# Kernel optimization log

Hardware: AMD Instinct MI355X
Metric: run time of the kernel (lower is better)

Reference implementation:

```python
import jax, jax.numpy as jnp
import numpy as np

NUM_HEADS = 32
NUM_KV_HEADS = 8
HEAD_DIM = 128
HIDDEN = 4096
ROPE_THETA = 10000.0
NEG = -1e9


def _split_heads(x, num_heads):
    b, s, _ = x.shape
    return x.reshape(b, s, num_heads, HEAD_DIM).transpose(0, 2, 1, 3)  # (B,H,S,D)


def _rope_cos_sin(position_ids, dtype):
    # position_ids: (B, S) int
    inv_freq = 1.0 / (ROPE_THETA ** (jnp.arange(0, HEAD_DIM, 2, dtype=jnp.float32) / HEAD_DIM))
    freqs = position_ids.astype(jnp.float32)[..., None] * inv_freq  # (B,S,D/2)
    emb = jnp.concatenate([freqs, freqs], axis=-1)  # (B,S,D)
    return jnp.cos(emb).astype(dtype)[:, None], jnp.sin(emb).astype(dtype)[:, None]  # (B,1,S,D)


def _rotate_half(x):
    x1, x2 = jnp.split(x, 2, axis=-1)
    return jnp.concatenate([-x2, x1], axis=-1)


def setup_inputs() -> dict:
    key = jax.random.key(0)
    ks = jax.random.split(key, 6)
    B, S = 1, 2048
    hidden_states = jax.random.normal(ks[0], (B, S, HIDDEN), dtype=jnp.float32)
    # additive causal mask: 0 on/below diagonal, NEG above
    causal = jnp.triu(jnp.full((S, S), NEG, dtype=jnp.float32), k=1)
    attention_mask = jnp.broadcast_to(causal, (B, 1, S, S))
    position_ids = jnp.broadcast_to(jnp.arange(S, dtype=jnp.int32), (B, S))
    sd = 1.0 / np.sqrt(HIDDEN)
    Wq = jax.random.normal(ks[1], (HIDDEN, NUM_HEADS * HEAD_DIM), dtype=jnp.float32) * sd
    Wk = jax.random.normal(ks[2], (HIDDEN, NUM_KV_HEADS * HEAD_DIM), dtype=jnp.float32) * sd
    Wv = jax.random.normal(ks[3], (HIDDEN, NUM_KV_HEADS * HEAD_DIM), dtype=jnp.float32) * sd
    Wo = jax.random.normal(ks[4], (NUM_HEADS * HEAD_DIM, HIDDEN), dtype=jnp.float32) * sd
    return {"hidden_states": hidden_states, "attention_mask": attention_mask,
            "position_ids": position_ids, "Wq": Wq, "Wk": Wk, "Wv": Wv, "Wo": Wo}


def reference(hidden_states, attention_mask, position_ids, Wq, Wk, Wv, Wo):
    groups = NUM_HEADS // NUM_KV_HEADS
    scale = HEAD_DIM ** (-0.5)
    q = _split_heads(hidden_states @ Wq, NUM_HEADS)        # (B,H,S,D)
    k = _split_heads(hidden_states @ Wk, NUM_KV_HEADS)     # (B,Hkv,S,D)
    v = _split_heads(hidden_states @ Wv, NUM_KV_HEADS)
    cos, sin = _rope_cos_sin(position_ids, q.dtype)
    q = q * cos + _rotate_half(q) * sin
    k = k * cos + _rotate_half(k) * sin
    # repeat_kv (faithful to tf.repeat along head axis)
    k = jnp.repeat(k, groups, axis=1)                      # (B,H,S,D)
    v = jnp.repeat(v, groups, axis=1)
    attn = jnp.einsum('bhqd,bhkd->bhqk', q, k) * scale
    attn = attn + attention_mask.astype(attn.dtype)
    attn = jax.nn.softmax(attn.astype(jnp.float32), axis=-1).astype(q.dtype)
    out = jnp.einsum('bhqk,bhkd->bhqd', attn, v)           # (B,H,S,D)
    b, _, s, _ = out.shape
    out = out.transpose(0, 2, 1, 3).reshape(b, s, NUM_HEADS * HEAD_DIM)
    return out @ Wo
```

## Files before the change

kernel.cpp:

```cpp
#include <hip/hip_runtime.h>
#include <math.h>

#define S_LEN 2048
#define HIDDEN 4096
#define NUM_HEADS 32
#define NUM_KV_HEADS 8
#define HEAD_DIM 128
#define NEG (-1e9f)

using short8 = __attribute__((ext_vector_type(8))) short;
using f32x4 = __attribute__((ext_vector_type(4))) float;

__device__ inline unsigned short f2bf(float f) {
  union { float f; unsigned u; } c;
  c.f = f;
  unsigned r = c.u + 0x7fffu + ((c.u >> 16) & 1u);
  return (unsigned short)(r >> 16);
}
__device__ inline float bf2f(unsigned short h) {
  union { unsigned u; float f; } c;
  c.u = ((unsigned)h) << 16;
  return c.f;
}
__device__ inline void gload16(const void* g, void* l) {
  __builtin_amdgcn_global_load_lds(
      (const __attribute__((address_space(1))) unsigned*)g,
      (__attribute__((address_space(3))) unsigned*)l, 16, 0, 0);
}

__global__ __launch_bounds__(256) void split_mat(const float* __restrict__ X,
                                                 unsigned short* __restrict__ Xh,
                                                 unsigned short* __restrict__ Xl,
                                                 int n4) {
  const int i = blockIdx.x * 256 + threadIdx.x;
  if (i >= n4) return;
  const float4 x = *reinterpret_cast<const float4*>(&X[(size_t)i * 4]);
  ushort4 h, l;
  h.x = f2bf(x.x); l.x = f2bf(x.x - bf2f(h.x));
  h.y = f2bf(x.y); l.y = f2bf(x.y - bf2f(h.y));
  h.z = f2bf(x.z); l.z = f2bf(x.z - bf2f(h.z));
  h.w = f2bf(x.w); l.w = f2bf(x.w - bf2f(h.w));
  *reinterpret_cast<ushort4*>(&Xh[(size_t)i * 4]) = h;
  *reinterpret_cast<ushort4*>(&Xl[(size_t)i * 4]) = l;
}

__global__ __launch_bounds__(256) void split_transpose(
    const float* __restrict__ B, unsigned short* __restrict__ Th,
    unsigned short* __restrict__ Tl, int K, int N) {
  __shared__ float ts[32][33];
  const int t = threadIdx.x;
  const int k0 = blockIdx.y * 32, n0 = blockIdx.x * 32;
  const int r = t >> 3, c4 = (t & 7) << 2;
  const float4 x = *reinterpret_cast<const float4*>(&B[(size_t)(k0 + r) * N + n0 + c4]);
  ts[r][c4 + 0] = x.x;
  ts[r][c4 + 1] = x.y;
  ts[r][c4 + 2] = x.z;
  ts[r][c4 + 3] = x.w;
  __syncthreads();
  const int col = r, ks = c4;
  ushort4 h, l;
#pragma unroll
  for (int e = 0; e < 4; ++e) {
    const float v = ts[ks + e][col];
    const unsigned short hh = f2bf(v);
    const unsigned short ll = f2bf(v - bf2f(hh));
    ((unsigned short*)&h)[e] = hh;
    ((unsigned short*)&l)[e] = ll;
  }
  *reinterpret_cast<ushort4*>(&Th[(size_t)(n0 + col) * K + k0 + ks]) = h;
  *reinterpret_cast<ushort4*>(&Tl[(size_t)(n0 + col) * K + k0 + ks]) = l;
}

#define BM 128
#define BN 128
#define BK 32

__global__ __launch_bounds__(256) void gemm_split(
    const unsigned short* __restrict__ Ah, const unsigned short* __restrict__ Al,
    const unsigned short* __restrict__ Bh, const unsigned short* __restrict__ Bl,
    float* __restrict__ C, int M, int N, int K) {
  __shared__ unsigned short sAh[BM * BK];
  __shared__ unsigned short sAl[BM * BK];
  __shared__ unsigned short sBh[BN * BK];
  __shared__ unsigned short sBl[BN * BK];

  const int t = threadIdx.x;
  const int lane = t & 63;
  const int w = t >> 6;
  const int bm = blockIdx.y * BM;
  const int bn = blockIdx.x * BN;
  const int wr = (w >> 1) * 64;
  const int wc = (w & 1) * 64;

  f32x4 acc[4][4] = {};

  const int lrow = lane & 15;
  const int kg = (lane >> 4) * 8;

  for (int k0 = 0; k0 < K; k0 += BK) {
    __syncthreads();
#pragma unroll
    for (int cc = 0; cc < 2; ++cc) {
      const int c = t + cc * 256;
      const int row = c >> 2, kk = (c & 3) * 8;
      const size_t ga = (size_t)(bm + row) * K + k0 + kk;
      const size_t gb = (size_t)(bn + row) * K + k0 + kk;
      gload16(Ah + ga, &sAh[c * 8]);
      gload16(Al + ga, &sAl[c * 8]);
      gload16(Bh + gb, &sBh[c * 8]);
      gload16(Bl + gb, &sBl[c * 8]);
    }
    __syncthreads();

    short8 ah[4], al[4], bh[4], bl[4];
#pragma unroll
    for (int i = 0; i < 4; ++i) {
      const int ar = (wr + i * 16 + lrow) * BK + kg;
      ah[i] = *reinterpret_cast<const short8*>(&sAh[ar]);
      al[i] = *reinterpret_cast<const short8*>(&sAl[ar]);
      const int br = (wc + i * 16 + lrow) * BK + kg;
      bh[i] = *reinterpret_cast<const short8*>(&sBh[br]);
      bl[i] = *reinterpret_cast<const short8*>(&sBl[br]);
    }
#pragma unroll
    for (int i = 0; i < 4; ++i)
#pragma unroll
      for (int j = 0; j < 4; ++j) {
        acc[i][j] = __builtin_amdgcn_mfma_f32_16x16x32_bf16(ah[i], bh[j], acc[i][j], 0, 0, 0);
        acc[i][j] = __builtin_amdgcn_mfma_f32_16x16x32_bf16(ah[i], bl[j], acc[i][j], 0, 0, 0);
        acc[i][j] = __builtin_amdgcn_mfma_f32_16x16x32_bf16(al[i], bh[j], acc[i][j], 0, 0, 0);
      }
  }

#pragma unroll
  for (int i = 0; i < 4; ++i) {
    const int row0 = bm + wr + i * 16 + (lane >> 4) * 4;
#pragma unroll
    for (int j = 0; j < 4; ++j) {
      const int col = bn + wc + j * 16 + (lane & 15);
#pragma unroll
      for (int r = 0; r < 4; ++r)
        C[(size_t)(row0 + r) * N + col] = acc[i][j][r];
    }
  }
}

__global__ void rope_convert(const float* __restrict__ q, const float* __restrict__ k,
                             const int* __restrict__ pos_ids,
                             unsigned short* __restrict__ Qh, unsigned short* __restrict__ Ql,
                             unsigned short* __restrict__ Kh, unsigned short* __restrict__ Kl) {
  const int idx = blockIdx.x * 256 + threadIdx.x;
  const int d = idx & 63;
  const int rest = idx >> 6;
  const int head = rest % (NUM_HEADS + NUM_KV_HEADS);
  const int s = rest / (NUM_HEADS + NUM_KV_HEADS);
  if (s >= S_LEN) return;

  const float pos = (float)pos_ids[s];
  const float inv = powf(10000.0f, -(float)d / 64.0f);
  const float ang = pos * inv;
  const float c = cosf(ang);
  const float sn = sinf(ang);

  if (head < NUM_HEADS) {
    const size_t b = (size_t)s * (NUM_HEADS * HEAD_DIM) + head * HEAD_DIM;
    const float x1 = q[b + d], x2 = q[b + d + 64];
    const float y1 = x1 * c - x2 * sn;
    const float y2 = x2 * c + x1 * sn;
    const unsigned short h1 = f2bf(y1), h2 = f2bf(y2);
    Qh[b + d] = h1;       Ql[b + d] = f2bf(y1 - bf2f(h1));
    Qh[b + d + 64] = h2;  Ql[b + d + 64] = f2bf(y2 - bf2f(h2));
  } else {
    const size_t b = (size_t)s * (NUM_KV_HEADS * HEAD_DIM) + (head - NUM_HEADS) * HEAD_DIM;
    const float x1 = k[b + d], x2 = k[b + d + 64];
    const float y1 = x1 * c - x2 * sn;
    const float y2 = x2 * c + x1 * sn;
    const unsigned short h1 = f2bf(y1), h2 = f2bf(y2);
    Kh[b + d] = h1;       Kl[b + d] = f2bf(y1 - bf2f(h1));
    Kh[b + d + 64] = h2;  Kl[b + d + 64] = f2bf(y2 - bf2f(h2));
  }
}

#define KSTR 136
#define VSTR 72

__global__ __launch_bounds__(256, 2) void attn_mfma(
    const unsigned short* __restrict__ Qh, const unsigned short* __restrict__ Ql,
    const unsigned short* __restrict__ Kh, const unsigned short* __restrict__ Kl,
    const unsigned short* __restrict__ Vth, const unsigned short* __restrict__ Vtl,
    float* __restrict__ O) {
  __shared__ unsigned short sKh[64 * KSTR];
  __shared__ unsigned short sKl[64 * KSTR];
  __shared__ unsigned short sVh[128 * VSTR];
  __shared__ unsigned short sVl[128 * VSTR];
  __shared__ unsigned short sP[64 * VSTR];

  const int qb = 31 - blockIdx.x;
  const int h = blockIdx.y;
  const int hk = h >> 2;
  const int t = threadIdx.x;
  const int lane = t & 63;
  const int w = t >> 6;
  const int lr = lane & 15;
  const int kg = (lane >> 4) * 8;

  short8 qa_h[4], qa_l[4];
  {
    const size_t qoff = (size_t)(qb * 64 + w * 16 + lr) * (NUM_HEADS * HEAD_DIM) + h * HEAD_DIM;
#pragma unroll
    for (int ks = 0; ks < 4; ++ks) {
      qa_h[ks] = *reinterpret_cast<const short8*>(&Qh[qoff + ks * 32 + kg]);
      qa_l[ks] = *reinterpret_cast<const short8*>(&Ql[qoff + ks * 32 + kg]);
    }
  }

  f32x4 acc_o[8] = {};
  float m_r[4], l_r[4];
#pragma unroll
  for (int r = 0; r < 4; ++r) { m_r[r] = -3.0e38f; l_r[r] = 0.0f; }

  const float scale = 0.08838834764831845f;

  for (int kt = 0; kt <= qb; ++kt) {
    __syncthreads();
#pragma unroll
    for (int i = 0; i < 4; ++i) {
      const int c = i * 256 + t;
      const int row = c >> 4, c8 = (c & 15) << 3;
      const size_t g = (size_t)(kt * 64 + row) * (NUM_KV_HEADS * HEAD_DIM) + hk * HEAD_DIM + c8;
      *reinterpret_cast<short8*>(&sKh[row * KSTR + c8]) =
          *reinterpret_cast<const short8*>(&Kh[g]);
      *reinterpret_cast<short8*>(&sKl[row * KSTR + c8]) =
          *reinterpret_cast<const short8*>(&Kl[g]);
    }
#pragma unroll
    for (int i = 0; i < 4; ++i) {
      const int c = i * 256 + t;
      const int d = c >> 3, c8 = (c & 7) << 3;
      const size_t g = (size_t)(hk * HEAD_DIM + d) * S_LEN + kt * 64 + c8;
      *reinterpret_cast<short8*>(&sVh[d * VSTR + c8]) =
          *reinterpret_cast<const short8*>(&Vth[g]);
      *reinterpret_cast<short8*>(&sVl[d * VSTR + c8]) =
          *reinterpret_cast<const short8*>(&Vtl[g]);
    }
    __syncthreads();

    f32x4 s_acc[4] = {};
#pragma unroll
    for (int j = 0; j < 4; ++j) {
      short8 kb_h[4], kb_l[4];
#pragma unroll
      for (int ks = 0; ks < 4; ++ks) {
        const int off = (j * 16 + lr) * KSTR + ks * 32 + kg;
        kb_h[ks] = *reinterpret_cast<const short8*>(&sKh[off]);
        kb_l[ks] = *reinterpret_cast<const short8*>(&sKl[off]);
      }
#pragma unroll
      for (int ks = 0; ks < 4; ++ks) {
        s_acc[j] = __builtin_amdgcn_mfma_f32_16x16x32_bf16(qa_h[ks], kb_h[ks], s_acc[j], 0, 0, 0);
        s_acc[j] = __builtin_amdgcn_mfma_f32_16x16x32_bf16(qa_h[ks], kb_l[ks], s_acc[j], 0, 0, 0);
        s_acc[j] = __builtin_amdgcn_mfma_f32_16x16x32_bf16(qa_l[ks], kb_h[ks], s_acc[j], 0, 0, 0);
      }
    }

    const bool last = (kt == qb);
#pragma unroll
    for (int r = 0; r < 4; ++r) {
      const int qg = qb * 64 + w * 16 + (lane >> 4) * 4 + r;
      float sc[4];
#pragma unroll
      for (int j = 0; j < 4; ++j) sc[j] = s_acc[j][r] * scale;
      if (last) {
#pragma unroll
        for (int j = 0; j < 4; ++j) {
          const int kgl = kt * 64 + j * 16 + lr;
          if (kgl > qg) sc[j] += NEG;
        }
      }
      float mx = fmaxf(fmaxf(sc[0], sc[1]), fmaxf(sc[2], sc[3]));
#pragma unroll
      for (int off = 1; off < 16; off <<= 1) mx = fmaxf(mx, __shfl_xor(mx, off, 16));
      const float mnew = fmaxf(m_r[r], mx);
      float p[4], su = 0.0f;
#pragma unroll
      for (int j = 0; j < 4; ++j) { p[j] = __expf(sc[j] - mnew); su += p[j]; }
#pragma unroll
      for (int off = 1; off < 16; off <<= 1) su += __shfl_xor(su, off, 16);
      const float rs = __expf(m_r[r] - mnew);
      l_r[r] = l_r[r] * rs + su;
      m_r[r] = mnew;
#pragma unroll
      for (int df = 0; df < 8; ++df) acc_o[df][r] *= rs;
      const int prow = (w * 16 + (lane >> 4) * 4 + r) * VSTR;
#pragma unroll
      for (int j = 0; j < 4; ++j) sP[prow + j * 16 + lr] = f2bf(p[j]);
    }
    __syncthreads();

    short8 pa[2];
#pragma unroll
    for (int ks = 0; ks < 2; ++ks)
      pa[ks] = *reinterpret_cast<const short8*>(&sP[(w * 16 + lr) * VSTR + ks * 32 + kg]);
#pragma unroll
    for (int df = 0; df < 8; ++df) {
#pragma unroll
      for (int ks = 0; ks < 2; ++ks) {
        const int off = (df * 16 + lr) * VSTR + ks * 32 + kg;
        const short8 vb_h = *reinterpret_cast<const short8*>(&sVh[off]);
        const short8 vb_l = *reinterpret_cast<const short8*>(&sVl[off]);
        acc_o[df] = __builtin_amdgcn_mfma_f32_16x16x32_bf16(pa[ks], vb_h, acc_o[df], 0, 0, 0);
        acc_o[df] = __builtin_amdgcn_mfma_f32_16x16x32_bf16(pa[ks], vb_l, acc_o[df], 0, 0, 0);
      }
    }
  }

#pragma unroll
  for (int r = 0; r < 4; ++r) {
    const int row = qb * 64 + w * 16 + (lane >> 4) * 4 + r;
    const float inv = 1.0f / l_r[r];
#pragma unroll
    for (int df = 0; df < 8; ++df)
      O[(size_t)row * (NUM_HEADS * HEAD_DIM) + h * HEAD_DIM + df * 16 + lr] =
          acc_o[df][r] * inv;
  }
}

#define TM 64
#define TN 64
#define TK 16

__global__ __launch_bounds__(256) void gemm_f32(const float* __restrict__ A,
                                                const float* __restrict__ B,
                                                float* __restrict__ C,
                                                int M, int N, int K) {
  __shared__ float As[TK][TM + 1];
  __shared__ float Bs[TK][TN + 1];
  const int t = threadIdx.x;
  const int bm = blockIdx.y * TM;
  const int bn = blockIdx.x * TN;
  const int tx = t & 15, ty = t >> 4;
  float acc[4][4] = {};
  for (int k0 = 0; k0 < K; k0 += TK) {
    {
      const int row = t >> 2;
      const int c4 = (t & 3) << 2;
      const float4 a4 = *reinterpret_cast<const float4*>(&A[(size_t)(bm + row) * K + k0 + c4]);
      As[c4 + 0][row] = a4.x; As[c4 + 1][row] = a4.y;
      As[c4 + 2][row] = a4.z; As[c4 + 3][row] = a4.w;
    }
    {
      const int row = t >> 4;
      const int c4 = (t & 15) << 2;
      const float4 b4 = *reinterpret_cast<const float4*>(&B[(size_t)(k0 + row) * N + bn + c4]);
      Bs[row][c4 + 0] = b4.x; Bs[row][c4 + 1] = b4.y;
      Bs[row][c4 + 2] = b4.z; Bs[row][c4 + 3] = b4.w;
    }
    __syncthreads();
#pragma unroll
    for (int kk = 0; kk < TK; ++kk) {
      float a[4], b[4];
#pragma unroll
      for (int i = 0; i < 4; ++i) a[i] = As[kk][ty * 4 + i];
#pragma unroll
      for (int j = 0; j < 4; ++j) b[j] = Bs[kk][tx * 4 + j];
#pragma unroll
      for (int i = 0; i < 4; ++i)
#pragma unroll
        for (int j = 0; j < 4; ++j) acc[i][j] += a[i] * b[j];
    }
    __syncthreads();
  }
#pragma unroll
  for (int i = 0; i < 4; ++i) {
    const int row = bm + ty * 4 + i;
#pragma unroll
    for (int j = 0; j < 4; ++j)
      C[(size_t)row * N + bn + tx * 4 + j] = acc[i][j];
  }
}

__global__ void rope_kernel(float* __restrict__ q, float* __restrict__ k,
                            const int* __restrict__ pos_ids) {
  const int idx = blockIdx.x * 256 + threadIdx.x;
  const int d = idx & 63;
  const int rest = idx >> 6;
  const int head = rest % (NUM_HEADS + NUM_KV_HEADS);
  const int s = rest / (NUM_HEADS + NUM_KV_HEADS);
  if (s >= S_LEN) return;
  const float pos = (float)pos_ids[s];
  const float inv = powf(10000.0f, -(float)d / 64.0f);
  const float ang = pos * inv;
  const float c = cosf(ang);
  const float sn = sinf(ang);
  float* base = (head < NUM_HEADS)
                    ? (q + (size_t)s * (NUM_HEADS * HEAD_DIM) + head * HEAD_DIM)
                    : (k + (size_t)s * (NUM_KV_HEADS * HEAD_DIM) + (head - NUM_HEADS) * HEAD_DIM);
  const float x1 = base[d];
  const float x2 = base[d + 64];
  base[d] = x1 * c - x2 * sn;
  base[d + 64] = x2 * c + x1 * sn;
}

#define QB 64
#define KT 32
#define PD 132

__global__ __launch_bounds__(256) void attn_kernel(
    const float* __restrict__ Q, const float* __restrict__ K,
    const float* __restrict__ V, float* __restrict__ O) {
  __shared__ float Qs[QB][PD];
  __shared__ float KVs[KT][PD];
  __shared__ float Ps[QB][KT + 2];
  const int qb = blockIdx.x;
  const int h = blockIdx.y;
  const int hk = h >> 2;
  const int t = threadIdx.x;
  const int tx = t & 15, ty = t >> 4;
#pragma unroll
  for (int r = 0; r < 8; ++r) {
    const int idx = r * 256 + t;
    const int row = idx >> 5;
    const int c4 = (idx & 31) << 2;
    *reinterpret_cast<float4*>(&Qs[row][c4]) = *reinterpret_cast<const float4*>(
        &Q[(size_t)(qb * QB + row) * (NUM_HEADS * HEAD_DIM) + h * HEAD_DIM + c4]);
  }
  float acc[4][8] = {};
  float mrow[4], lrow[4];
#pragma unroll
  for (int i = 0; i < 4; ++i) { mrow[i] = -3.0e38f; lrow[i] = 0.0f; }
  const float scale = 0.08838834764831845f;
  const int ktiles = 2 * qb + 2;
  for (int kt = 0; kt < ktiles; ++kt) {
    __syncthreads();
#pragma unroll
    for (int r = 0; r < 4; ++r) {
      const int idx = r * 256 + t;
      const int row = idx >> 5;
      const int c4 = (idx & 31) << 2;
      *reinterpret_cast<float4*>(&KVs[row][c4]) = *reinterpret_cast<const float4*>(
          &K[(size_t)(kt * KT + row) * (NUM_KV_HEADS * HEAD_DIM) + hk * HEAD_DIM + c4]);
    }
    __syncthreads();
    float sc[4][2] = {};
    for (int d4 = 0; d4 < HEAD_DIM; d4 += 4) {
      float4 a[4], b[2];
#pragma unroll
      for (int i = 0; i < 4; ++i) a[i] = *reinterpret_cast<const float4*>(&Qs[ty * 4 + i][d4]);
#pragma unroll
      for (int j = 0; j < 2; ++j) b[j] = *reinterpret_cast<const float4*>(&KVs[tx * 2 + j][d4]);
#pragma unroll
      for (int i = 0; i < 4; ++i)
#pragma unroll
        for (int j = 0; j < 2; ++j)
          sc[i][j] += a[i].x * b[j].x + a[i].y * b[j].y + a[i].z * b[j].z + a[i].w * b[j].w;
    }
    const bool need_mask = (kt * KT + KT - 1) > (qb * QB);
#pragma unroll
    for (int i = 0; i < 4; ++i) {
      const int qg = qb * QB + ty * 4 + i;
#pragma unroll
      for (int j = 0; j < 2; ++j) {
        float v = sc[i][j] * scale;
        if (need_mask) {
          const int kgl = kt * KT + tx * 2 + j;
          if (kgl > qg) v += NEG;
        }
        sc[i][j] = v;
      }
    }
#pragma unroll
    for (int i = 0; i < 4; ++i) {
      float mx = fmaxf(sc[i][0], sc[i][1]);
#pragma unroll
      for (int off = 1; off < 16; off <<= 1) mx = fmaxf(mx, __shfl_xor(mx, off, 16));
      const float mnew = fmaxf(mrow[i], mx);
      const float p0 = __expf(sc[i][0] - mnew);
      const float p1 = __expf(sc[i][1] - mnew);
      float su = p0 + p1;
#pragma unroll
      for (int off = 1; off < 16; off <<= 1) su += __shfl_xor(su, off, 16);
      const float rsc = __expf(mrow[i] - mnew);
      lrow[i] = lrow[i] * rsc + su;
      mrow[i] = mnew;
#pragma unroll
      for (int j = 0; j < 8; ++j) acc[i][j] *= rsc;
      Ps[ty * 4 + i][tx * 2 + 0] = p0;
      Ps[ty * 4 + i][tx * 2 + 1] = p1;
    }
    __syncthreads();
#pragma unroll
    for (int r = 0; r < 4; ++r) {
      const int idx = r * 256 + t;
      const int row = idx >> 5;
      const int c4 = (idx & 31) << 2;
      *reinterpret_cast<float4*>(&KVs[row][c4]) = *reinterpret_cast<const float4*>(
          &V[(size_t)(kt * KT + row) * (NUM_KV_HEADS * HEAD_DIM) + hk * HEAD_DIM + c4]);
    }
    __syncthreads();
    for (int kk = 0; kk < KT; ++kk) {
      const float4 b0 = *reinterpret_cast<const float4*>(&KVs[kk][tx * 8]);
      const float4 b1 = *reinterpret_cast<const float4*>(&KVs[kk][tx * 8 + 4]);
#pragma unroll
      for (int i = 0; i < 4; ++i) {
        const float p = Ps[ty * 4 + i][kk];
        acc[i][0] += p * b0.x; acc[i][1] += p * b0.y;
        acc[i][2] += p * b0.z; acc[i][3] += p * b0.w;
        acc[i][4] += p * b1.x; acc[i][5] += p * b1.y;
        acc[i][6] += p * b1.z; acc[i][7] += p * b1.w;
      }
    }
  }
#pragma unroll
  for (int i = 0; i < 4; ++i) {
    const int row = qb * QB + ty * 4 + i;
    const float inv = 1.0f / lrow[i];
#pragma unroll
    for (int j = 0; j < 8; ++j)
      O[(size_t)row * (NUM_HEADS * HEAD_DIM) + h * HEAD_DIM + tx * 8 + j] = acc[i][j] * inv;
  }
}

extern "C" void kernel_launch(void* const* d_in, const int* in_sizes, int n_in,
                              void* d_out, int out_size, void* d_ws,
                              size_t ws_size, hipStream_t stream) {
  const float* hidden = (const float*)d_in[0];
  const int* pos_ids = (const int*)d_in[2];
  const float* Wq = (const float*)d_in[3];
  const float* Wk = (const float*)d_in[4];
  const float* Wv = (const float*)d_in[5];
  const float* Wo = (const float*)d_in[6];
  float* out = (float*)d_out;

  char* ws = (char*)d_ws;
  const size_t SZ_Q = (size_t)S_LEN * HIDDEN * 4;
  const size_t SZ_KV = (size_t)S_LEN * 1024 * 4;
  const size_t SZ_AH = (size_t)S_LEN * HIDDEN * 2;
  const size_t SZ_WH = (size_t)HIDDEN * HIDDEN * 2;
  const size_t MB = (size_t)1 << 20;

  float* q = (float*)(ws);
  float* k = (float*)(ws + SZ_Q);
  float* v = (float*)(ws + SZ_Q + SZ_KV);
  float* ao_fb = (float*)(ws + SZ_Q + 2 * SZ_KV);
  unsigned short* Ah = (unsigned short*)(ws + 2 * SZ_Q + 2 * SZ_KV);
  unsigned short* Al = (unsigned short*)(ws + 2 * SZ_Q + 2 * SZ_KV + SZ_AH);
  char* whbase = ws + 2 * SZ_Q + 2 * SZ_KV + 2 * SZ_AH;
  unsigned short* Wh = (unsigned short*)(whbase);
  unsigned short* Wl = (unsigned short*)(whbase + SZ_WH);
  const size_t needed = 2 * SZ_Q + 2 * SZ_KV + 2 * SZ_AH + 2 * SZ_WH;

  unsigned short* Qhb = Ah;
  unsigned short* Qlb = Al;
  unsigned short* Khb = (unsigned short*)(whbase);
  unsigned short* Klb = (unsigned short*)(whbase + 4 * MB);
  unsigned short* Vth = (unsigned short*)(whbase + 8 * MB);
  unsigned short* Vtl = (unsigned short*)(whbase + 12 * MB);
  float* ao = q;

  if (ws_size >= needed) {
    const int n4_hidden = S_LEN * HIDDEN / 4;
    split_mat<<<(n4_hidden + 255) / 256, 256, 0, stream>>>(hidden, Ah, Al, n4_hidden);
    split_transpose<<<dim3(HIDDEN / 32, HIDDEN / 32), 256, 0, stream>>>(Wq, Wh, Wl, HIDDEN, HIDDEN);
    gemm_split<<<dim3(HIDDEN / BN, S_LEN / BM), 256, 0, stream>>>(Ah, Al, Wh, Wl, q, S_LEN, HIDDEN, HIDDEN);
    split_transpose<<<dim3(1024 / 32, HIDDEN / 32), 256, 0, stream>>>(Wk, Wh, Wl, HIDDEN, 1024);
    gemm_split<<<dim3(1024 / BN, S_LEN / BM), 256, 0, stream>>>(Ah, Al, Wh, Wl, k, S_LEN, 1024, HIDDEN);
    split_transpose<<<dim3(1024 / 32, HIDDEN / 32), 256, 0, stream>>>(Wv, Wh, Wl, HIDDEN, 1024);
    gemm_split<<<dim3(1024 / BN, S_LEN / BM), 256, 0, stream>>>(Ah, Al, Wh, Wl, v, S_LEN, 1024, HIDDEN);

    {
      const int total = S_LEN * (NUM_HEADS + NUM_KV_HEADS) * 64;
      rope_convert<<<(total + 255) / 256, 256, 0, stream>>>(q, k, pos_ids, Qhb, Qlb, Khb, Klb);
    }
    split_transpose<<<dim3(1024 / 32, S_LEN / 32), 256, 0, stream>>>(v, Vth, Vtl, S_LEN, 1024);

    attn_mfma<<<dim3(32, NUM_HEADS), 256, 0, stream>>>(Qhb, Qlb, Khb, Klb, Vth, Vtl, ao);

    split_mat<<<(n4_hidden + 255) / 256, 256, 0, stream>>>(ao, Ah, Al, n4_hidden);
    split_transpose<<<dim3(HIDDEN / 32, HIDDEN / 32), 256, 0, stream>>>(Wo, Wh, Wl, HIDDEN, HIDDEN);
    gemm_split<<<dim3(HIDDEN / BN, S_LEN / BM), 256, 0, stream>>>(Ah, Al, Wh, Wl, out, S_LEN, HIDDEN, HIDDEN);
  } else {
    gemm_f32<<<dim3(HIDDEN / TN, S_LEN / TM), 256, 0, stream>>>(hidden, Wq, q, S_LEN, HIDDEN, HIDDEN);
    gemm_f32<<<dim3(1024 / TN, S_LEN / TM), 256, 0, stream>>>(hidden, Wk, k, S_LEN, 1024, HIDDEN);
    gemm_f32<<<dim3(1024 / TN, S_LEN / TM), 256, 0, stream>>>(hidden, Wv, v, S_LEN, 1024, HIDDEN);
    {
      const int total = S_LEN * (NUM_HEADS + NUM_KV_HEADS) * 64;
      rope_kernel<<<(total + 255) / 256, 256, 0, stream>>>(q, k, pos_ids);
    }
    attn_kernel<<<dim3(S_LEN / QB, NUM_HEADS), 256, 0, stream>>>(q, k, v, ao_fb);
    gemm_f32<<<dim3(HIDDEN / TN, S_LEN / TM), 256, 0, stream>>>(ao_fb, Wo, out, S_LEN, HIDDEN, HIDDEN);
  }
}
```

Before: 1.241 ms.

## Fuse K and V projections into one GEMM and split P instead of V

The K and V weight matrices are split-transposed into one contiguous buffer so a single 2048-wide split-bf16 GEMM computes K and V together, replacing two narrower launches. RoPE and the V transpose now read K and V from the combined buffer with a row stride. In attention, the low-order bf16 part now comes from the softmax probabilities P instead of from V. This drops the V-low global and LDS loads while keeping two MFMAs per step, at the cost of extra conversion work and LDS stores for P and reduced precision on V.

```diff
diff --git a/kernel.cpp b/kernel.cpp
--- a/kernel.cpp
+++ b/kernel.cpp
@@ -46,12 +46,12 @@
 
 __global__ __launch_bounds__(256) void split_transpose(
     const float* __restrict__ B, unsigned short* __restrict__ Th,
-    unsigned short* __restrict__ Tl, int K, int N) {
+    unsigned short* __restrict__ Tl, int K, int N, int ldb) {
   __shared__ float ts[32][33];
   const int t = threadIdx.x;
   const int k0 = blockIdx.y * 32, n0 = blockIdx.x * 32;
   const int r = t >> 3, c4 = (t & 7) << 2;
-  const float4 x = *reinterpret_cast<const float4*>(&B[(size_t)(k0 + r) * N + n0 + c4]);
+  const float4 x = *reinterpret_cast<const float4*>(&B[(size_t)(k0 + r) * ldb + n0 + c4]);
   ts[r][c4 + 0] = x.x;
   ts[r][c4 + 1] = x.y;
   ts[r][c4 + 2] = x.z;
@@ -145,8 +145,8 @@
   }
 }
 
-__global__ void rope_convert(const float* __restrict__ q, const float* __restrict__ k,
-                             const int* __restrict__ pos_ids,
+__global__ void rope_convert(const float* __restrict__ q, const float* __restrict__ kv,
+                             int kld, const int* __restrict__ pos_ids,
                              unsigned short* __restrict__ Qh, unsigned short* __restrict__ Ql,
                              unsigned short* __restrict__ Kh, unsigned short* __restrict__ Kl) {
   const int idx = blockIdx.x * 256 + threadIdx.x;
@@ -171,8 +171,10 @@
     Qh[b + d] = h1;       Ql[b + d] = f2bf(y1 - bf2f(h1));
     Qh[b + d + 64] = h2;  Ql[b + d + 64] = f2bf(y2 - bf2f(h2));
   } else {
-    const size_t b = (size_t)s * (NUM_KV_HEADS * HEAD_DIM) + (head - NUM_HEADS) * HEAD_DIM;
-    const float x1 = k[b + d], x2 = k[b + d + 64];
+    const int kh = head - NUM_HEADS;
+    const size_t gsrc = (size_t)s * kld + kh * HEAD_DIM;
+    const size_t b = (size_t)s * (NUM_KV_HEADS * HEAD_DIM) + kh * HEAD_DIM;
+    const float x1 = kv[gsrc + d], x2 = kv[gsrc + d + 64];
     const float y1 = x1 * c - x2 * sn;
     const float y2 = x2 * c + x1 * sn;
     const unsigned short h1 = f2bf(y1), h2 = f2bf(y2);
@@ -187,13 +189,12 @@
 __global__ __launch_bounds__(256, 2) void attn_mfma(
     const unsigned short* __restrict__ Qh, const unsigned short* __restrict__ Ql,
     const unsigned short* __restrict__ Kh, const unsigned short* __restrict__ Kl,
-    const unsigned short* __restrict__ Vth, const unsigned short* __restrict__ Vtl,
-    float* __restrict__ O) {
+    const unsigned short* __restrict__ Vth, float* __restrict__ O) {
   __shared__ unsigned short sKh[64 * KSTR];
   __shared__ unsigned short sKl[64 * KSTR];
   __shared__ unsigned short sVh[128 * VSTR];
-  __shared__ unsigned short sVl[128 * VSTR];
-  __shared__ unsigned short sP[64 * VSTR];
+  __shared__ unsigned short sPh[64 * VSTR];
+  __shared__ unsigned short sPl[64 * VSTR];
 
   const int qb = 31 - blockIdx.x;
   const int h = blockIdx.y;
@@ -240,8 +241,6 @@
       const size_t g = (size_t)(hk * HEAD_DIM + d) * S_LEN + kt * 64 + c8;
       *reinterpret_cast<short8*>(&sVh[d * VSTR + c8]) =
           *reinterpret_cast<const short8*>(&Vth[g]);
-      *reinterpret_cast<short8*>(&sVl[d * VSTR + c8]) =
-          *reinterpret_cast<const short8*>(&Vtl[g]);
     }
     __syncthreads();
 
@@ -293,23 +292,29 @@
       for (int df = 0; df < 8; ++df) acc_o[df][r] *= rs;
       const int prow = (w * 16 + (lane >> 4) * 4 + r) * VSTR;
 #pragma unroll
-      for (int j = 0; j < 4; ++j) sP[prow + j * 16 + lr] = f2bf(p[j]);
-    }
-    __syncthreads();
-
-    short8 pa[2];
-#pragma unroll
-    for (int ks = 0; ks < 2; ++ks)
-      pa[ks] = *reinterpret_cast<const short8*>(&sP[(w * 16 + lr) * VSTR + ks * 32 + kg]);
+      for (int j = 0; j < 4; ++j) {
+        const unsigned short ph = f2bf(p[j]);
+        sPh[prow + j * 16 + lr] = ph;
+        sPl[prow + j * 16 + lr] = f2bf(p[j] - bf2f(ph));
+      }
+    }
+    __syncthreads();
+
+    short8 pa_h[2], pa_l[2];
+#pragma unroll
+    for (int ks = 0; ks < 2; ++ks) {
+      const int off = (w * 16 + lr) * VSTR + ks * 32 + kg;
+      pa_h[ks] = *reinterpret_cast<const short8*>(&sPh[off]);
+      pa_l[ks] = *reinterpret_cast<const short8*>(&sPl[off]);
+    }
 #pragma unroll
     for (int df = 0; df < 8; ++df) {
 #pragma unroll
       for (int ks = 0; ks < 2; ++ks) {
         const int off = (df * 16 + lr) * VSTR + ks * 32 + kg;
-        const short8 vb_h = *reinterpret_cast<const short8*>(&sVh[off]);
-        const short8 vb_l = *reinterpret_cast<const short8*>(&sVl[off]);
-        acc_o[df] = __builtin_amdgcn_mfma_f32_16x16x32_bf16(pa[ks], vb_h, acc_o[df], 0, 0, 0);
-        acc_o[df] = __builtin_amdgcn_mfma_f32_16x16x32_bf16(pa[ks], vb_l, acc_o[df], 0, 0, 0);
+        const short8 vb = *reinterpret_cast<const short8*>(&sVh[off]);
+        acc_o[df] = __builtin_amdgcn_mfma_f32_16x16x32_bf16(pa_h[ks], vb, acc_o[df], 0, 0, 0);
+        acc_o[df] = __builtin_amdgcn_mfma_f32_16x16x32_bf16(pa_l[ks], vb, acc_o[df], 0, 0, 0);
       }
     }
   }
@@ -532,61 +537,66 @@
   float* out = (float*)d_out;
 
   char* ws = (char*)d_ws;
+  const size_t MB = (size_t)1 << 20;
   const size_t SZ_Q = (size_t)S_LEN * HIDDEN * 4;
   const size_t SZ_KV = (size_t)S_LEN * 1024 * 4;
   const size_t SZ_AH = (size_t)S_LEN * HIDDEN * 2;
   const size_t SZ_WH = (size_t)HIDDEN * HIDDEN * 2;
-  const size_t MB = (size_t)1 << 20;
+  const size_t needed = 2 * SZ_Q + 2 * SZ_KV + 2 * SZ_AH + 2 * SZ_WH;
 
   float* q = (float*)(ws);
-  float* k = (float*)(ws + SZ_Q);
-  float* v = (float*)(ws + SZ_Q + SZ_KV);
-  float* ao_fb = (float*)(ws + SZ_Q + 2 * SZ_KV);
-  unsigned short* Ah = (unsigned short*)(ws + 2 * SZ_Q + 2 * SZ_KV);
-  unsigned short* Al = (unsigned short*)(ws + 2 * SZ_Q + 2 * SZ_KV + SZ_AH);
-  char* whbase = ws + 2 * SZ_Q + 2 * SZ_KV + 2 * SZ_AH;
+  float* kv = (float*)(ws + 32 * MB);
+  float* ao = (float*)(ws + 48 * MB);
+  unsigned short* Ah = (unsigned short*)(ws + 80 * MB);
+  unsigned short* Al = (unsigned short*)(ws + 96 * MB);
+  char* whbase = ws + 112 * MB;
   unsigned short* Wh = (unsigned short*)(whbase);
   unsigned short* Wl = (unsigned short*)(whbase + SZ_WH);
-  const size_t needed = 2 * SZ_Q + 2 * SZ_KV + 2 * SZ_AH + 2 * SZ_WH;
-
+  unsigned short* Wkvh = (unsigned short*)(whbase);
+  unsigned short* Wkvl = (unsigned short*)(whbase + 16 * MB);
   unsigned short* Qhb = Ah;
   unsigned short* Qlb = Al;
   unsigned short* Khb = (unsigned short*)(whbase);
   unsigned short* Klb = (unsigned short*)(whbase + 4 * MB);
   unsigned short* Vth = (unsigned short*)(whbase + 8 * MB);
   unsigned short* Vtl = (unsigned short*)(whbase + 12 * MB);
-  float* ao = q;
+
+  float* k_fb = (float*)(ws + SZ_Q);
+  float* v_fb = (float*)(ws + SZ_Q + SZ_KV);
+  float* ao_fb = (float*)(ws + SZ_Q + 2 * SZ_KV);
 
   if (ws_size >= needed) {
     const int n4_hidden = S_LEN * HIDDEN / 4;
     split_mat<<<(n4_hidden + 255) / 256, 256, 0, stream>>>(hidden, Ah, Al, n4_hidden);
-    split_transpose<<<dim3(HIDDEN / 32, HIDDEN / 32), 256, 0, stream>>>(Wq, Wh, Wl, HIDDEN, HIDDEN);
+
+    split_transpose<<<dim3(HIDDEN / 32, HIDDEN / 32), 256, 0, stream>>>(Wq, Wh, Wl, HIDDEN, HIDDEN, HIDDEN);
     gemm_split<<<dim3(HIDDEN / BN, S_LEN / BM), 256, 0, stream>>>(Ah, Al, Wh, Wl, q, S_LEN, HIDDEN, HIDDEN);
-    split_transpose<<<dim3(1024 / 32, HIDDEN / 32), 256, 0, stream>>>(Wk, Wh, Wl, HIDDEN, 1024);
-    gemm_split<<<dim3(1024 / BN, S_LEN / BM), 256, 0, stream>>>(Ah, Al, Wh, Wl, k, S_LEN, 1024, HIDDEN);
-    split_transpose<<<dim3(1024 / 32, HIDDEN / 32), 256, 0, stream>>>(Wv, Wh, Wl, HIDDEN, 1024);
-    gemm_split<<<dim3(1024 / BN, S_LEN / BM), 256, 0, stream>>>(Ah, Al, Wh, Wl, v, S_LEN, 1024, HIDDEN);
+
+    split_transpose<<<dim3(1024 / 32, HIDDEN / 32), 256, 0, stream>>>(Wk, Wkvh, Wkvl, HIDDEN, 1024, 1024);
+    split_transpose<<<dim3(1024 / 32, HIDDEN / 32), 256, 0, stream>>>(
+        Wv, Wkvh + (size_t)1024 * HIDDEN, Wkvl + (size_t)1024 * HIDDEN, HIDDEN, 1024, 1024);
+    gemm_split<<<dim3(2048 / BN, S_LEN / BM), 256, 0, stream>>>(Ah, Al, Wkvh, Wkvl, kv, S_LEN, 2048, HIDDEN);
 
     {
       const int total = S_LEN * (NUM_HEADS + NUM_KV_HEADS) * 64;
-      rope_convert<<<(total + 255) / 256, 256, 0, stream>>>(q, k, pos_ids, Qhb, Qlb, Khb, Klb);
-    }
-    split_transpose<<<dim3(1024 / 32, S_LEN / 32), 256, 0, stream>>>(v, Vth, Vtl, S_LEN, 1024);
-
-    attn_mfma<<<dim3(32, NUM_HEADS), 256, 0, stream>>>(Qhb, Qlb, Khb, Klb, Vth, Vtl, ao);
+      rope_convert<<<(total + 255) / 256, 256, 0, stream>>>(q, kv, 2048, pos_ids, Qhb, Qlb, Khb, Klb);
+    }
+    split_transpose<<<dim3(1024 / 32, S_LEN / 32), 256, 0, stream>>>(kv + 1024, Vth, Vtl, S_LEN, 1024, 2048);
+
+    attn_mfma<<<dim3(32, NUM_HEADS), 256, 0, stream>>>(Qhb, Qlb, Khb, Klb, Vth, ao);
 
     split_mat<<<(n4_hidden + 255) / 256, 256, 0, stream>>>(ao, Ah, Al, n4_hidden);
-    split_transpose<<<dim3(HIDDEN / 32, HIDDEN / 32), 256, 0, stream>>>(Wo, Wh, Wl, HIDDEN, HIDDEN);
+    split_transpose<<<dim3(HIDDEN / 32, HIDDEN / 32), 256, 0, stream>>>(Wo, Wh, Wl, HIDDEN, HIDDEN, HIDDEN);
     gemm_split<<<dim3(HIDDEN / BN, S_LEN / BM), 256, 0, stream>>>(Ah, Al, Wh, Wl, out, S_LEN, HIDDEN, HIDDEN);
   } else {
     gemm_f32<<<dim3(HIDDEN / TN, S_LEN / TM), 256, 0, stream>>>(hidden, Wq, q, S_LEN, HIDDEN, HIDDEN);
-    gemm_f32<<<dim3(1024 / TN, S_LEN / TM), 256, 0, stream>>>(hidden, Wk, k, S_LEN, 1024, HIDDEN);
-    gemm_f32<<<dim3(1024 / TN, S_LEN / TM), 256, 0, stream>>>(hidden, Wv, v, S_LEN, 1024, HIDDEN);
+    gemm_f32<<<dim3(1024 / TN, S_LEN / TM), 256, 0, stream>>>(hidden, Wk, k_fb, S_LEN, 1024, HIDDEN);
+    gemm_f32<<<dim3(1024 / TN, S_LEN / TM), 256, 0, stream>>>(hidden, Wv, v_fb, S_LEN, 1024, HIDDEN);
     {
       const int total = S_LEN * (NUM_HEADS + NUM_KV_HEADS) * 64;
-      rope_kernel<<<(total + 255) / 256, 256, 0, stream>>>(q, k, pos_ids);
-    }
-    attn_kernel<<<dim3(S_LEN / QB, NUM_HEADS), 256, 0, stream>>>(q, k, v, ao_fb);
+      rope_kernel<<<(total + 255) / 256, 256, 0, stream>>>(q, k_fb, pos_ids);
+    }
+    attn_kernel<<<dim3(S_LEN / QB, NUM_HEADS), 256, 0, stream>>>(q, k_fb, v_fb, ao_fb);
     gemm_f32<<<dim3(HIDDEN / TN, S_LEN / TM), 256, 0, stream>>>(ao_fb, Wo, out, S_LEN, HIDDEN, HIDDEN);
   }
 }
```

Result: faster. 1.078 ms (-13.1%).
